# Kernel tuning notes

Measured on AMD Instinct MI355X. Metric: run time of the kernel, lower is better.

## Reference

```python
import jax, jax.numpy as jnp
import numpy as np

VX, VY = 0.2, 0.2
X_OFF = VX / 2 + 0.0          # vx/2 + pc_range[0]
Y_OFF = VY / 2 + (-40.0)      # vy/2 + pc_range[1]
K = 8                          # hardcoded in GCNLayer
BN_EPS = 1e-3
LRELU_SLOPE = 0.2
V, T, C_IN, C_OUT = 4096, 100, 4, 64


def _gcn_layer(x, conv_w, bn_gamma, bn_beta, bn_mean, bn_var):
    """DGCNN EdgeConv layer. x: [N, T, C]. Returns [N, T, O]."""
    N, Tn, C = x.shape
    # KNN on negative squared distance (self included in topk, as in torch code)
    xx = jnp.sum(x * x, axis=-1)                       # [N, T]
    inner = jnp.einsum('ntc,nsc->nts', x, x)           # [N, T, T]
    neg_dist = 2.0 * inner - xx[:, :, None] - xx[:, None, :]
    _, idx = jax.lax.top_k(neg_dist, K)                # [N, T, K]
    # gather neighbor features: nbr[n,t,k,c] = x[n, idx[n,t,k], c]
    nbr = x[jnp.arange(N)[:, None, None], idx]         # [N, T, K, C]
    xc = x[:, :, None, :]                              # [N, T, 1, C]
    edge = jnp.concatenate(
        [nbr - xc, jnp.broadcast_to(xc, (N, Tn, K, C))], axis=-1)  # [N,T,K,2C]
    # 1x1 conv (no bias) + eval-mode BatchNorm + LeakyReLU(0.2)
    h = jnp.einsum('ntkc,oc->ntko', edge, conv_w)      # [N, T, K, O]
    scale = bn_gamma / jnp.sqrt(bn_var + BN_EPS)
    h = (h - bn_mean) * scale + bn_beta
    h = jax.nn.leaky_relu(h, LRELU_SLOPE)
    return jnp.max(h, axis=2)                          # max over k -> [N, T, O]


def setup_inputs() -> dict:
    key = jax.random.key(0)
    k1, k2, k3, k4, k5, k6 = jax.random.split(key, 6)
    features = jax.random.normal(k1, (V, T, C_IN), dtype=jnp.float32)
    num_voxels = jnp.maximum(
        jax.random.randint(k2, (V,), 0, T), 1).astype(jnp.int32)
    coors = jax.random.randint(k3, (V, 4), 0, 352).astype(jnp.int32)
    # GCNLayer params: Conv2d(18, 64, 1, bias=False) + BatchNorm2d(64)
    conv_w = jax.random.normal(k4, (C_OUT, 18), dtype=jnp.float32) * 0.1
    bn_gamma = jnp.ones((C_OUT,), jnp.float32)
    bn_beta = jnp.zeros((C_OUT,), jnp.float32)
    bn_mean = jax.random.normal(k5, (C_OUT,), jnp.float32) * 0.1
    bn_var = 1.0 + 0.1 * jax.random.uniform(k6, (C_OUT,), jnp.float32)
    return {"features": features, "conv_w": conv_w, "bn_gamma": bn_gamma,
            "bn_beta": bn_beta, "bn_mean": bn_mean, "bn_var": bn_var,
            "num_voxels": num_voxels, "coors": coors}


def reference(features, conv_w, bn_gamma, bn_beta, bn_mean, bn_var,
              num_voxels, coors):
    nv = num_voxels.astype(features.dtype)
    # decorate: cluster offsets (xyz - mean) and pillar-center offsets (xy)
    points_mean = jnp.sum(features[:, :, :3], axis=1, keepdims=True) / nv[:, None, None]
    f_cluster = features[:, :, :3] - points_mean                      # [V,T,3]
    fx = features[:, :, 0] - (coors[:, 3].astype(features.dtype)[:, None] * VX + X_OFF)
    fy = features[:, :, 1] - (coors[:, 2].astype(features.dtype)[:, None] * VY + Y_OFF)
    f_center = jnp.stack([fx, fy], axis=-1)                           # [V,T,2]
    feat = jnp.concatenate([features, f_cluster, f_center], axis=-1)  # [V,T,9]
    # padding mask: point t valid iff t < num_voxels[v]
    mask = (jnp.arange(T)[None, :] < num_voxels[:, None]).astype(features.dtype)
    feat = feat * mask[:, :, None]
    # single GCN (last) layer; batch_process chunking is a no-op mathematically
    out = _gcn_layer(feat, conv_w, bn_gamma, bn_beta, bn_mean, bn_var)  # [V,T,64]
    out = out * mask[:, :, None]            # (+ zeros prev_features_out)
    out = jnp.max(out, axis=1)              # max over points -> [V, 64]
    return out
```

## Files before the change

### kernel.cpp

```cpp
#include <hip/hip_runtime.h>

#define TPTS 100
#define CO   64
#define KK   8

__device__ __forceinline__ unsigned umin_(unsigned a, unsigned b) { return a < b ? a : b; }
__device__ __forceinline__ unsigned umax_(unsigned a, unsigned b) { return a > b ? a : b; }

__device__ __forceinline__ unsigned dist_key(const float4 qt, const float4 qs, unsigned s) {
    float dx = qt.x - qs.x, dy = qt.y - qs.y;
    float dz = qt.z - qs.z, dw = qt.w - qs.w;
    float e = __fmaf_rn(dx, dx, __fmaf_rn(dy, dy, __fmaf_rn(dz, dz, dw * dw)));
    return (__float_as_uint(e) & 0xFFFFFF80u) | s;
}

__device__ __forceinline__ void ins8(unsigned val[KK], unsigned key) {
    #pragma unroll
    for (int k = KK - 1; k >= 1; --k)
        val[k] = umin_(val[k], umax_(val[k - 1], key));
    val[0] = umin_(val[0], key);
}

__global__ __launch_bounds__(256) void dgcnn_kernel(
    const float* __restrict__ features,
    const float* __restrict__ conv_w,
    const float* __restrict__ bn_gamma,
    const float* __restrict__ bn_beta,
    const float* __restrict__ bn_mean,
    const float* __restrict__ bn_var,
    const int*  __restrict__ num_voxels,
    const int*  __restrict__ coors,
    float* __restrict__ out)
{
    __shared__ float s_feat[TPTS][12];
    __shared__ float s_xx[TPTS];
    __shared__ int   s_idx[KK][TPTS];
    __shared__ float s_red[4][CO];
    __shared__ float s_mean[4];
    __shared__ union {
        float stage[TPTS][4];
        float g[TPTS][CO];
    } s_u;

    const float INF = __builtin_inff();
    const int v   = blockIdx.x;
    const int tid = threadIdx.x;
    const int nv  = num_voxels[v];

    float4 f = make_float4(0.f, 0.f, 0.f, 0.f);
    if (tid < TPTS) {
        f = reinterpret_cast<const float4*>(features)[v * TPTS + tid];
        *reinterpret_cast<float4*>(&s_u.stage[tid][0]) = f;
    }
    __syncthreads();

    if (tid < 96) {
        int ch = tid >> 5, j = tid & 31;
        float p = s_u.stage[j][ch] + s_u.stage[j + 32][ch] + s_u.stage[j + 64][ch];
        if (j < 4) p += s_u.stage[j + 96][ch];
        #pragma unroll
        for (int off = 16; off >= 1; off >>= 1)
            p += __shfl_xor(p, off, 32);
        if (j == 0) s_mean[ch] = p / (float)nv;
    }
    __syncthreads();

    if (tid < TPTS) {
        float mask = (tid < nv) ? 1.0f : 0.0f;
        float c3 = (float)coors[v * 4 + 3];
        float c2 = (float)coors[v * 4 + 2];
        float r0 = f.x * mask, r1 = f.y * mask, r2 = f.z * mask, r3 = f.w * mask;
        float r4 = (f.x - s_mean[0]) * mask;
        float r5 = (f.y - s_mean[1]) * mask;
        float r6 = (f.z - s_mean[2]) * mask;
        float r7 = (f.x - (c3 * 0.2f + 0.1f)) * mask;
        float r8 = (f.y - (c2 * 0.2f - 39.9f)) * mask;
        float xx = r0*r0 + r1*r1 + r2*r2 + r3*r3 + r4*r4
                 + r5*r5 + r6*r6 + r7*r7 + r8*r8;
        float4* rowv = reinterpret_cast<float4*>(&s_feat[tid][0]);
        rowv[0] = make_float4(1.7320508075688772f * r0,
                              1.7320508075688772f * r1,
                              1.4142135623730951f * r2, r3);
        rowv[1] = make_float4(r4, r5, r6, r7);
        rowv[2] = make_float4(r8, 0.f, 0.f, 0.f);
        s_xx[tid] = xx;
    }

    const int o = tid & 63;
    const int w = tid >> 6;
    const float sgn = (bn_gamma[o] < 0.f) ? -1.f : 1.f;
    float w1[9], w2[9];
    #pragma unroll
    for (int c = 0; c < 9; ++c) {
        const float ws = (c == 0 || c == 1) ? 0.57735026918962576f
                       : (c == 2) ? 0.70710678118654752f : 1.f;
        float a = conv_w[o * 18 + c];
        float b = conv_w[o * 18 + 9 + c];
        w1[c] = a * sgn * ws;
        w2[c] = (b - a) * sgn * ws;
    }
    __syncthreads();

    const int side = tid >> 7;
    const int t    = tid & 127;
    unsigned val[KK];
    if (t < nv) {
        const float4 qt = *reinterpret_cast<const float4*>(&s_feat[t][0]);
        #pragma unroll
        for (int k = 0; k < KK; ++k) val[k] = 0xFFFFFFFFu;
        const int h  = (nv + 1) >> 1;
        const int lo = side ? h : 0;
        const int hi = side ? nv : h;
        #pragma unroll 2
        for (int s = lo; s < hi; ++s) {
            const float4 qs = *reinterpret_cast<const float4*>(&s_feat[s][0]);
            ins8(val, dist_key(qt, qs, (unsigned)s));
        }
        if (side) {
            int mcnt = TPTS - nv; if (mcnt > KK) mcnt = KK;
            unsigned kmb = __float_as_uint(s_xx[t]) & 0xFFFFFF80u;
            for (int j = 0; j < mcnt; ++j)
                ins8(val, kmb | (unsigned)(nv + j));
        } else {
            #pragma unroll
            for (int k = 0; k < KK; ++k) s_idx[k][t] = (int)val[k];
        }
    }
    __syncthreads();

    if (side && t < nv) {
        unsigned a[KK];
        #pragma unroll
        for (int k = 0; k < KK; ++k) a[k] = (unsigned)s_idx[k][t];
        #pragma unroll
        for (int k = 0; k < KK; ++k)
            s_idx[k][t] = (int)(umin_(a[k], val[KK - 1 - k]) & 127u);
    }

    {
        int r0 = nv + w, r1 = nv + w + 4;
        if (r0 < TPTS) s_u.g[r0][o] = 0.f;
        if (r1 < TPTS) s_u.g[r1][o] = 0.f;
    }

    for (int sR = w; sR < nv; sR += 4) {
        const float4* row = reinterpret_cast<const float4*>(&s_feat[sR][0]);
        float4 a = row[0], b = row[1];
        float c8 = s_feat[sR][8];
        float g = a.x * w1[0];
        g = __fmaf_rn(a.y, w1[1], g);
        g = __fmaf_rn(a.z, w1[2], g);
        g = __fmaf_rn(a.w, w1[3], g);
        g = __fmaf_rn(b.x, w1[4], g);
        g = __fmaf_rn(b.y, w1[5], g);
        g = __fmaf_rn(b.z, w1[6], g);
        g = __fmaf_rn(b.w, w1[7], g);
        g = __fmaf_rn(c8,  w1[8], g);
        s_u.g[sR][o] = g;
    }
    __syncthreads();

    float acc = -INF;
    for (int tt = w; tt < nv; tt += 4) {
        const float4* row = reinterpret_cast<const float4*>(&s_feat[tt][0]);
        float4 a = row[0], b = row[1];
        float c8 = s_feat[tt][8];
        float base = a.x * w2[0];
        base = __fmaf_rn(a.y, w2[1], base);
        base = __fmaf_rn(a.z, w2[2], base);
        base = __fmaf_rn(a.w, w2[3], base);
        base = __fmaf_rn(b.x, w2[4], base);
        base = __fmaf_rn(b.y, w2[5], base);
        base = __fmaf_rn(b.z, w2[6], base);
        base = __fmaf_rn(b.w, w2[7], base);
        base = __fmaf_rn(c8,  w2[8], base);
        int i0 = s_idx[0][tt], i1 = s_idx[1][tt], i2 = s_idx[2][tt], i3 = s_idx[3][tt];
        int i4 = s_idx[4][tt], i5 = s_idx[5][tt], i6 = s_idx[6][tt], i7 = s_idx[7][tt];
        float g0 = s_u.g[i0][o], g1 = s_u.g[i1][o], g2 = s_u.g[i2][o], g3 = s_u.g[i3][o];
        float g4 = s_u.g[i4][o], g5 = s_u.g[i5][o], g6 = s_u.g[i6][o], g7 = s_u.g[i7][o];
        float gm = fmaxf(fmaxf(fmaxf(g0, g1), fmaxf(g2, g3)),
                         fmaxf(fmaxf(g4, g5), fmaxf(g6, g7)));
        acc = fmaxf(acc, gm + base);
    }
    s_red[w][o] = acc;
    __syncthreads();

    if (tid < CO) {
        float m = fmaxf(fmaxf(s_red[0][tid], s_red[1][tid]),
                        fmaxf(s_red[2][tid], s_red[3][tid]));
        float scale = bn_gamma[tid] / sqrtf(bn_var[tid] + 0.001f);
        float bias  = bn_beta[tid] - bn_mean[tid] * scale;
        float h = m * fabsf(scale) + bias;
        float a = (h > 0.f) ? h : 0.2f * h;
        if (nv < TPTS) a = fmaxf(a, 0.f);
        out[v * CO + tid] = a;
    }
}

extern "C" void kernel_launch(void* const* d_in, const int* in_sizes, int n_in,
                              void* d_out, int out_size, void* d_ws, size_t ws_size,
                              hipStream_t stream) {
    const float* features = (const float*)d_in[0];
    const float* conv_w   = (const float*)d_in[1];
    const float* bn_gamma = (const float*)d_in[2];
    const float* bn_beta  = (const float*)d_in[3];
    const float* bn_mean  = (const float*)d_in[4];
    const float* bn_var   = (const float*)d_in[5];
    const int*   num_vox  = (const int*)d_in[6];
    const int*   coor     = (const int*)d_in[7];
    float* outp = (float*)d_out;
    const int V = in_sizes[6];
    dgcnn_kernel<<<V, 256, 0, stream>>>(features, conv_w, bn_gamma, bn_beta,
                                        bn_mean, bn_var, num_vox, coor, outp);
}
```

Before: 117.2 us.

## Split KNN scan within a wave and merge halves via shuffle, pack indices

```diff
diff --git a/kernel.cpp b/kernel.cpp
--- a/kernel.cpp
+++ b/kernel.cpp
@@ -32,11 +32,11 @@
     const int*  __restrict__ coors,
     float* __restrict__ out)
 {
-    __shared__ float s_feat[TPTS][12];
-    __shared__ float s_xx[TPTS];
-    __shared__ int   s_idx[KK][TPTS];
-    __shared__ float s_red[4][CO];
-    __shared__ float s_mean[4];
+    __shared__ float    s_feat[TPTS][12];
+    __shared__ float    s_xx[TPTS];
+    __shared__ unsigned s_idxp[TPTS][2];
+    __shared__ float    s_red[4][CO];
+    __shared__ float    s_mean[4];
     __shared__ union {
         float stage[TPTS][4];
         float g[TPTS][CO];
@@ -86,8 +86,8 @@
         s_xx[tid] = xx;
     }
 
-    const int o = tid & 63;
-    const int w = tid >> 6;
+    const int o  = tid & 63;
+    const int wv = tid >> 6;
     const float sgn = (bn_gamma[o] < 0.f) ? -1.f : 1.f;
     float w1[9], w2[9];
     #pragma unroll
@@ -101,49 +101,50 @@
     }
     __syncthreads();
 
-    const int side = tid >> 7;
-    const int t    = tid & 127;
-    unsigned val[KK];
-    if (t < nv) {
-        const float4 qt = *reinterpret_cast<const float4*>(&s_feat[t][0]);
-        #pragma unroll
-        for (int k = 0; k < KK; ++k) val[k] = 0xFFFFFFFFu;
-        const int h  = (nv + 1) >> 1;
-        const int lo = side ? h : 0;
-        const int hi = side ? nv : h;
-        #pragma unroll 2
-        for (int s = lo; s < hi; ++s) {
-            const float4 qs = *reinterpret_cast<const float4*>(&s_feat[s][0]);
-            ins8(val, dist_key(qt, qs, (unsigned)s));
+    if (wv * 32 < nv) {
+        const int trow = wv * 32 + (o & 31);
+        const int bsd  = o >> 5;
+        if (trow < nv) {
+            const float4 qt = *reinterpret_cast<const float4*>(&s_feat[trow][0]);
+            unsigned val[KK];
+            #pragma unroll
+            for (int k = 0; k < KK; ++k) val[k] = 0xFFFFFFFFu;
+            const int h  = (nv + 1) >> 1;
+            int s        = bsd ? h  : 0;
+            const int se = bsd ? nv : h;
+            #pragma unroll 2
+            for (; s < se; ++s) {
+                const float4 qs = *reinterpret_cast<const float4*>(&s_feat[s][0]);
+                ins8(val, dist_key(qt, qs, (unsigned)s));
+            }
+            if (bsd) {
+                int mcnt = TPTS - nv; if (mcnt > KK) mcnt = KK;
+                unsigned kmb = __float_as_uint(s_xx[trow]) & 0xFFFFFF80u;
+                for (int j = 0; j < mcnt; ++j)
+                    ins8(val, kmb | (unsigned)(nv + j));
+            }
+            unsigned other[KK];
+            #pragma unroll
+            for (int k = 0; k < KK; ++k) other[k] = __shfl_xor(val[k], 32);
+            if (!bsd) {
+                unsigned m[KK];
+                #pragma unroll
+                for (int k = 0; k < KK; ++k)
+                    m[k] = umin_(val[k], other[KK - 1 - k]) & 127u;
+                unsigned p0 = m[0] | (m[1] << 8) | (m[2] << 16) | (m[3] << 24);
+                unsigned p1 = m[4] | (m[5] << 8) | (m[6] << 16) | (m[7] << 24);
+                *reinterpret_cast<uint2*>(&s_idxp[trow][0]) = make_uint2(p0, p1);
+            }
         }
-        if (side) {
-            int mcnt = TPTS - nv; if (mcnt > KK) mcnt = KK;
-            unsigned kmb = __float_as_uint(s_xx[t]) & 0xFFFFFF80u;
-            for (int j = 0; j < mcnt; ++j)
-                ins8(val, kmb | (unsigned)(nv + j));
-        } else {
-            #pragma unroll
-            for (int k = 0; k < KK; ++k) s_idx[k][t] = (int)val[k];
-        }
-    }
-    __syncthreads();
-
-    if (side && t < nv) {
-        unsigned a[KK];
-        #pragma unroll
-        for (int k = 0; k < KK; ++k) a[k] = (unsigned)s_idx[k][t];
-        #pragma unroll
-        for (int k = 0; k < KK; ++k)
-            s_idx[k][t] = (int)(umin_(a[k], val[KK - 1 - k]) & 127u);
     }
 
     {
-        int r0 = nv + w, r1 = nv + w + 4;
+        int r0 = nv + wv, r1 = nv + wv + 4;
         if (r0 < TPTS) s_u.g[r0][o] = 0.f;
         if (r1 < TPTS) s_u.g[r1][o] = 0.f;
     }
 
-    for (int sR = w; sR < nv; sR += 4) {
+    for (int sR = wv; sR < nv; sR += 4) {
         const float4* row = reinterpret_cast<const float4*>(&s_feat[sR][0]);
         float4 a = row[0], b = row[1];
         float c8 = s_feat[sR][8];
@@ -161,7 +162,7 @@
     __syncthreads();
 
     float acc = -INF;
-    for (int tt = w; tt < nv; tt += 4) {
+    for (int tt = wv; tt < nv; tt += 4) {
         const float4* row = reinterpret_cast<const float4*>(&s_feat[tt][0]);
         float4 a = row[0], b = row[1];
         float c8 = s_feat[tt][8];
@@ -174,15 +175,18 @@
         base = __fmaf_rn(b.z, w2[6], base);
         base = __fmaf_rn(b.w, w2[7], base);
         base = __fmaf_rn(c8,  w2[8], base);
-        int i0 = s_idx[0][tt], i1 = s_idx[1][tt], i2 = s_idx[2][tt], i3 = s_idx[3][tt];
-        int i4 = s_idx[4][tt], i5 = s_idx[5][tt], i6 = s_idx[6][tt], i7 = s_idx[7][tt];
+        uint2 pk = *reinterpret_cast<const uint2*>(&s_idxp[tt][0]);
+        int i0 =  pk.x        & 255, i1 = (pk.x >>  8) & 255;
+        int i2 = (pk.x >> 16) & 255, i3 = (pk.x >> 24) & 255;
+        int i4 =  pk.y        & 255, i5 = (pk.y >>  8) & 255;
+        int i6 = (pk.y >> 16) & 255, i7 = (pk.y >> 24) & 255;
         float g0 = s_u.g[i0][o], g1 = s_u.g[i1][o], g2 = s_u.g[i2][o], g3 = s_u.g[i3][o];
         float g4 = s_u.g[i4][o], g5 = s_u.g[i5][o], g6 = s_u.g[i6][o], g7 = s_u.g[i7][o];
         float gm = fmaxf(fmaxf(fmaxf(g0, g1), fmaxf(g2, g3)),
                          fmaxf(fmaxf(g4, g5), fmaxf(g6, g7)));
         acc = fmaxf(acc, gm + base);
     }
-    s_red[w][o] = acc;
+    s_red[wv][o] = acc;
     __syncthreads();
 
     if (tid < CO) {
```

New measurement: 118.8 us. No clear change (+1.3%).
